# Performance work log

Hardware: AMD Instinct MI355X
Metric: run time of the kernel (lower is better)

## Reference

```python
import jax, jax.numpy as jnp
import numpy as np

B, T, C, H = 1, 2048, 1024, 16
HD = C // H
WIN = 256            # sliding_window_size
NLEV = 256           # quantization levels (input/weights/output)
CLAMP = 1.0          # clamping bounds [-1, 1] when quantization is active


def window_mask(n_tokens, win):
    i = jnp.arange(n_tokens)[:, None]
    j = jnp.arange(n_tokens)[None, :]
    return ((j <= i) & (j > i - win)).astype(jnp.float32)  # [T, T]


def quantize_ste(x, n_levels, vmin, vmax):
    # quantization_custom: q_step * round(x / q_step), straight-through gradient
    q_step = (vmax - vmin) / (n_levels - 1)
    q = q_step * jnp.round(x / q_step)
    return x + jax.lax.stop_gradient(q - x)


def setup_inputs() -> dict:
    key = jax.random.key(0)
    k0, k1, k2 = jax.random.split(key, 3)
    x = jax.random.normal(k0, (B, T, C), dtype=jnp.float32)
    w_attn = jax.random.normal(k1, (C, 3 * C), dtype=jnp.float32) * 0.02  # c_attn.weight (no bias)
    w_proj = jax.random.normal(k2, (C, C), dtype=jnp.float32) * 0.02      # c_proj.weight (no bias)
    return {"x": x, "w_attn": w_attn, "w_proj": w_proj}


def reference(x, w_attn, w_proj):
    # c_attn + split into per-head q,k,v -> [B,H,T,HD]
    qkv = x @ w_attn
    q, k, v = jnp.split(qkv, 3, axis=-1)
    to_heads = lambda t: t.reshape(B, T, H, HD).transpose(0, 2, 1, 3)
    q, k, v = to_heads(q), to_heads(k), to_heads(v)

    # range_scalers are identity here (a=1, b=0, not trainable); clamp + quantize (DAC simulation)
    q = quantize_ste(jnp.clip(q, -CLAMP, CLAMP), NLEV, -CLAMP, CLAMP)
    k = quantize_ste(jnp.clip(k, -CLAMP, CLAMP), NLEV, -CLAMP, CLAMP)
    v = quantize_ste(jnp.clip(v, -CLAMP, CLAMP), NLEV, -CLAMP, CLAMP)

    mask = window_mask(T, WIN)  # [T, T]

    # similarity = matmul: [B,H,T,T]
    att = jnp.einsum('bhqd,bhkd->bhqk', q, k)
    # masked_fill with mask_value_1 = 0.0, decay = Identity
    att = jnp.where(mask == 0, 0.0, att)
    # att_score_scaler: a = HD**-0.5
    att = att * (HD ** -0.5)
    # output clamp + quantization of analog array readout
    att = quantize_ste(jnp.clip(att, -CLAMP, CLAMP), NLEV, -CLAMP, CLAMP)
    # masked_fill with mask_value_2 = -inf, then softmax (NL)
    att = jnp.where(mask == 0, -jnp.inf, att)
    att = jax.nn.softmax(att, axis=-1)

    # weight_average = matmul: [B,H,T,HD]
    y = jnp.einsum('bhqk,bhkd->bhqd', att, v)
    # weight_average_scaler identity; output clamp + quantize; output_scaler identity
    y = quantize_ste(jnp.clip(y, -CLAMP, CLAMP), NLEV, -CLAMP, CLAMP)

    y = y.transpose(0, 2, 1, 3).reshape(B, T, C)
    y = y @ w_proj  # resid dropout p=0.0
    return y
```

## Files before the change

kernel.cpp:

```cpp
#include <hip/hip_runtime.h>

using u16 = unsigned short;
using u32 = unsigned int;

typedef __bf16 bf16x8 __attribute__((ext_vector_type(8)));
typedef float f32x4 __attribute__((ext_vector_type(4)));

#define T_SEQ 2048
#define NC 1024
#define HDIM 64
#define WINSZ 256
#define QSTEP (2.0f / 255.0f)

__device__ __forceinline__ float b2f(u16 u) {
  u32 v = ((u32)u) << 16;
  return __builtin_bit_cast(float, v);
}
__device__ __forceinline__ u16 f2b(float f) {
  u32 x = __builtin_bit_cast(u32, f);
  u32 r = (x + 0x7fffu + ((x >> 16) & 1u)) >> 16;
  return (u16)r;
}
__device__ __forceinline__ float quantize(float v) {
  v = fminf(fmaxf(v, -1.0f), 1.0f);
  return QSTEP * rintf(v / QSTEP);
}

__global__ __launch_bounds__(256) void k1_prep(const float* __restrict__ x, u16* __restrict__ xb,
                                               const float* __restrict__ wa, u16* __restrict__ wTa,
                                               const float* __restrict__ wp, u16* __restrict__ wTp) {
  if (blockIdx.z == 2) {
    const int nb = gridDim.x * gridDim.y;
    const int bid = blockIdx.y * gridDim.x + blockIdx.x;
    const int n4 = T_SEQ * NC / 4;
    for (int i = bid * 256 + threadIdx.x; i < n4; i += nb * 256) {
      const float4 v = ((const float4*)x)[i];
      ushort4 o;
      o.x = f2b(v.x); o.y = f2b(v.y); o.z = f2b(v.z); o.w = f2b(v.w);
      ((ushort4*)xb)[i] = o;
    }
    return;
  }
  const int iswp = (blockIdx.z == 1);
  if (iswp && blockIdx.x >= 16) return;
  const float* in = iswp ? wp : wa;
  u16* out = iswp ? wTp : wTa;
  const int Cc = iswp ? 1024 : 3072;
  __shared__ u16 tile[64][65];
  const int tc = blockIdx.x * 64, tr = blockIdx.y * 64;
  const int lx = threadIdx.x & 63, ly = threadIdx.x >> 6;
#pragma unroll
  for (int r = ly; r < 64; r += 4)
    tile[r][lx] = f2b(in[(long)(tr + r) * Cc + tc + lx]);
  __syncthreads();
  const int e = threadIdx.x & 31;
  const int r0 = (threadIdx.x >> 5) & 1;
  const int w = threadIdx.x >> 6;
#pragma unroll
  for (int it = 0; it < 8; it++) {
    const int r = it * 8 + w * 2 + r0;
    ushort2 o2;
    o2.x = tile[2 * e][r];
    o2.y = tile[2 * e + 1][r];
    *(ushort2*)&out[(tc + r) * 1024 + tr + 2 * e] = o2;
  }
}

__global__ __launch_bounds__(256, 3) void k2_qkv(const u16* __restrict__ A,
                                                 const u16* __restrict__ BT,
                                                 u16* __restrict__ o0, u16* __restrict__ o1,
                                                 u16* __restrict__ o2) {
  __shared__ __align__(16) u16 As[2][4096];
  __shared__ __align__(16) u16 Bs[2][8192];
  const int tid = threadIdx.x;
  const int lane = tid & 63;
  const int wave = tid >> 6;
  const int wr = wave >> 1, wc = wave & 1;
  const int ln15 = lane & 15, lq = lane >> 4;
  const int l7 = ln15 & 7;

  const int wg = blockIdx.y * 24 + blockIdx.x;
  const int xcd = wg & 7, t = wg >> 3;
  const int bx = (xcd & 1) * 12 + t % 12;
  const int by = (xcd >> 1) * 8 + t / 12;
  const int m0 = by * 64, n0 = bx * 128;

  const int crow = tid >> 3, csl = tid & 7;
  const u16* ag0 = A + (m0 + crow) * NC + csl * 8;
  const u16* bg0 = BT + (n0 + crow) * NC + csl * 8;
  const int wofs = crow * 64 + (csl ^ (crow & 7)) * 8;

  uint4 pa0, pa1, pb0, pb1, pb2, pb3;
  uint4 qa0, qa1, qb0, qb1, qb2, qb3;
  f32x4 acc[2][4] = {};

#define K2_LOADP(KT)                                  \
  {                                                   \
    pa0 = *(const uint4*)(ag0 + (KT));                \
    pa1 = *(const uint4*)(ag0 + 32 * NC + (KT));      \
    pb0 = *(const uint4*)(bg0 + (KT));                \
    pb1 = *(const uint4*)(bg0 + 32 * NC + (KT));      \
    pb2 = *(const uint4*)(bg0 + 64 * NC + (KT));      \
    pb3 = *(const uint4*)(bg0 + 96 * NC + (KT));      \
  }
#define K2_LOADQ(KT)                                  \
  {                                                   \
    qa0 = *(const uint4*)(ag0 + (KT));                \
    qa1 = *(const uint4*)(ag0 + 32 * NC + (KT));      \
    qb0 = *(const uint4*)(bg0 + (KT));                \
    qb1 = *(const uint4*)(bg0 + 32 * NC + (KT));      \
    qb2 = *(const uint4*)(bg0 + 64 * NC + (KT));      \
    qb3 = *(const uint4*)(bg0 + 96 * NC + (KT));      \
  }
#define K2_WRITEP(BUF)                                \
  {                                                   \
    *(uint4*)&As[BUF][wofs] = pa0;                    \
    *(uint4*)&As[BUF][wofs + 2048] = pa1;             \
    *(uint4*)&Bs[BUF][wofs] = pb0;                    \
    *(uint4*)&Bs[BUF][wofs + 2048] = pb1;             \
    *(uint4*)&Bs[BUF][wofs + 4096] = pb2;             \
    *(uint4*)&Bs[BUF][wofs + 6144] = pb3;             \
  }
#define K2_WRITEQ(BUF)                                \
  {                                                   \
    *(uint4*)&As[BUF][wofs] = qa0;                    \
    *(uint4*)&As[BUF][wofs + 2048] = qa1;             \
    *(uint4*)&Bs[BUF][wofs] = qb0;                    \
    *(uint4*)&Bs[BUF][wofs + 2048] = qb1;             \
    *(uint4*)&Bs[BUF][wofs + 4096] = qb2;             \
    *(uint4*)&Bs[BUF][wofs + 6144] = qb3;             \
  }

  auto compute = [&](const u16* LA, const u16* LB) {
#pragma unroll
    for (int s = 0; s < 2; s++) {
      const int kc = s * 4 + lq;
      const int sw = kc ^ l7;
      bf16x8 af[2], bfr[4];
#pragma unroll
      for (int r = 0; r < 2; r++) {
        const int ar = wr * 32 + r * 16 + ln15;
        af[r] = *(const bf16x8*)&LA[(ar * 8 + sw) * 8];
      }
#pragma unroll
      for (int c = 0; c < 4; c++) {
        const int br = wc * 64 + c * 16 + ln15;
        bfr[c] = *(const bf16x8*)&LB[(br * 8 + sw) * 8];
      }
#pragma unroll
      for (int r = 0; r < 2; r++)
#pragma unroll
        for (int c = 0; c < 4; c++)
          acc[r][c] = __builtin_amdgcn_mfma_f32_16x16x32_bf16(af[r], bfr[c], acc[r][c], 0, 0, 0);
    }
  };

  K2_LOADP(0);
  K2_WRITEP(0);
  K2_LOADQ(64);

  for (int kt = 0; kt < NC; kt += 128) {
    __syncthreads();
    if (kt + 128 < NC) K2_LOADP(kt + 128);
    compute(As[0], Bs[0]);
    K2_WRITEQ(1);
    __syncthreads();
    if (kt + 192 < NC) K2_LOADQ(kt + 192);
    compute(As[1], Bs[1]);
    if (kt + 128 < NC) K2_WRITEP(0);
  }
#undef K2_LOADP
#undef K2_LOADQ
#undef K2_WRITEP
#undef K2_WRITEQ

#pragma unroll
  for (int c = 0; c < 4; c++) {
    const int gcol = n0 + wc * 64 + c * 16 + ln15;
    const int p = gcol >> 10;
    const int h = (gcol & 1023) >> 6;
    const int hd = gcol & 63;
#pragma unroll
    for (int r = 0; r < 2; r++) {
      const int rbase = m0 + wr * 32 + r * 16 + lq * 4;
#pragma unroll
      for (int g = 0; g < 4; g++) {
        const u16 b = f2b(quantize(acc[r][c][g]));
        const int row = rbase + g;
        if (p == 0)      o0[(h * T_SEQ + row) * HDIM + hd] = b;
        else if (p == 1) o1[(h * T_SEQ + row) * HDIM + hd] = b;
        else             o2[(h * HDIM + hd) * T_SEQ + row] = b;
      }
    }
  }
}

__global__ __launch_bounds__(256, 4) void k3_attn(const u16* __restrict__ qh,
                                                  const u16* __restrict__ kh,
                                                  const u16* __restrict__ vt,
                                                  u16* __restrict__ yq) {
  __shared__ __align__(16) u16 S[32 * 328];
  __shared__ float Linv[32];
  const int tid = threadIdx.x;
  const int lane = tid & 63;
  const int wave = tid >> 6;
  const int ln15 = lane & 15, lq = lane >> 4;

  const int g = blockIdx.y * 64 + blockIdx.x;
  const int lin = (g & 7) * 128 + (g >> 3);
  const int h = lin >> 6;
  const int i0 = (lin & 63) * 32;
  const int j0 = i0 - 256;

  const u16* qb = qh + (h * T_SEQ + i0) * HDIM;
  const u16* kb = kh + h * T_SEQ * HDIM;

  bf16x8 qf[2][2];
#pragma unroll
  for (int r = 0; r < 2; r++) {
    qf[r][0] = *(const bf16x8*)&qb[(r * 16 + ln15) * HDIM + lq * 8];
    qf[r][1] = *(const bf16x8*)&qb[(r * 16 + ln15) * HDIM + 32 + lq * 8];
  }

  bf16x8 kf[5][2];
#pragma unroll
  for (int t = 0; t < 5; t++) {
    const int jt = j0 + (wave + t * 4) * 16;
    if (jt >= 0 && jt <= T_SEQ - 16) {
      kf[t][0] = *(const bf16x8*)&kb[(jt + ln15) * HDIM + lq * 8];
      kf[t][1] = *(const bf16x8*)&kb[(jt + ln15) * HDIM + 32 + lq * 8];
    } else {
      kf[t][0] = bf16x8{};
      kf[t][1] = bf16x8{};
    }
  }

#pragma unroll
  for (int t = 0; t < 5; t++) {
    const int ct = wave + t * 4;
    const int jt = j0 + ct * 16;
#pragma unroll
    for (int rt = 0; rt < 2; rt++) {
      const bool skip = (ct < rt) || (ct > rt + 16) || (jt < 0);
      f32x4 s = {0.f, 0.f, 0.f, 0.f};
      if (!skip) {
        __builtin_amdgcn_s_setprio(1);
        s = __builtin_amdgcn_mfma_f32_16x16x32_bf16(kf[t][0], qf[rt][0], s, 0, 0, 0);
        s = __builtin_amdgcn_mfma_f32_16x16x32_bf16(kf[t][1], qf[rt][1], s, 0, 0, 0);
        __builtin_amdgcn_s_setprio(0);
      }
      const int i = i0 + rt * 16 + ln15;
      ushort4 pk;
      u16* pp = (u16*)&pk;
#pragma unroll
      for (int g2 = 0; g2 < 4; g2++) {
        const int j = jt + lq * 4 + g2;
        float v = -INFINITY;
        if (!skip && j <= i && j > i - WINSZ) v = quantize(s[g2] * 0.125f);
        pp[g2] = f2b(v);
      }
      *(ushort4*)&S[(rt * 16 + ln15) * 328 + ct * 16 + lq * 4] = pk;
    }
  }

  const u16* vb = vt + (h * HDIM + wave * 16 + ln15) * T_SEQ;
  bf16x8 vf[9];
#pragma unroll
  for (int kk = 0; kk < 9; kk++) {
    int jb = j0 + kk * 32 + lq * 8;
    if (jb < 0) jb = 0;
    vf[kk] = *(const bf16x8*)&vb[jb];
  }
  __syncthreads();

  {
    const int r = tid >> 3, sg = tid & 7;
    u16* Srow = &S[r * 328 + sg * 40];
    uint4 ch[5];
    float m = -INFINITY;
#pragma unroll
    for (int c = 0; c < 5; c++) {
      ch[c] = *(const uint4*)&Srow[c * 8];
      const u32* w = (const u32*)&ch[c];
#pragma unroll
      for (int d = 0; d < 4; d++) {
        m = fmaxf(m, b2f((u16)(w[d] & 0xffffu)));
        m = fmaxf(m, b2f((u16)(w[d] >> 16)));
      }
    }
    m = fmaxf(m, __shfl_xor(m, 1));
    m = fmaxf(m, __shfl_xor(m, 2));
    m = fmaxf(m, __shfl_xor(m, 4));
    float l = 0.0f;
#pragma unroll
    for (int c = 0; c < 5; c++) {
      u32* w = (u32*)&ch[c];
#pragma unroll
      for (int d = 0; d < 4; d++) {
        const float e0 = __expf(b2f((u16)(w[d] & 0xffffu)) - m);
        const float e1 = __expf(b2f((u16)(w[d] >> 16)) - m);
        l += e0 + e1;
        w[d] = ((u32)f2b(e1) << 16) | f2b(e0);
      }
      *(uint4*)&Srow[c * 8] = ch[c];
    }
    l += __shfl_xor(l, 1);
    l += __shfl_xor(l, 2);
    l += __shfl_xor(l, 4);
    if (sg == 0) Linv[r] = 1.0f / l;
  }
  __syncthreads();

  f32x4 acc[2] = {};
#pragma unroll
  for (int kk = 0; kk < 9; kk++) {
#pragma unroll
    for (int rt = 0; rt < 2; rt++) {
      const bf16x8 pf = *(const bf16x8*)&S[(rt * 16 + ln15) * 328 + kk * 32 + lq * 8];
      __builtin_amdgcn_s_setprio(1);
      acc[rt] = __builtin_amdgcn_mfma_f32_16x16x32_bf16(pf, vf[kk], acc[rt], 0, 0, 0);
      __builtin_amdgcn_s_setprio(0);
    }
  }
#pragma unroll
  for (int rt = 0; rt < 2; rt++)
#pragma unroll
    for (int g2 = 0; g2 < 4; g2++) {
      const int row = rt * 16 + lq * 4 + g2;
      const int i = i0 + row;
      yq[i * NC + h * HDIM + wave * 16 + ln15] = f2b(quantize(acc[rt][g2] * Linv[row]));
    }
}

__global__ __launch_bounds__(256, 4) void k4_proj(const u16* __restrict__ A,
                                                  const u16* __restrict__ BT,
                                                  float* __restrict__ of) {
  __shared__ __align__(16) u16 As[2][4096];
  __shared__ __align__(16) u16 Bs[2][4096];
  const int tid = threadIdx.x;
  const int lane = tid & 63;
  const int wave = tid >> 6;
  const int wr = wave >> 1, wc = wave & 1;
  const int ln15 = lane & 15, lq = lane >> 4;
  const int l7 = ln15 & 7;

  const int wg = blockIdx.y * 16 + blockIdx.x;
  const int xcd = wg & 7, t = wg >> 3;
  const int bx = (xcd & 1) * 8 + t % 8;
  const int by = (xcd >> 1) * 8 + t / 8;
  const int m0 = by * 64, n0 = bx * 64;

  const int crow = tid >> 3, csl = tid & 7;
  const u16* ag0 = A + (m0 + crow) * NC + csl * 8;
  const u16* bg0 = BT + (n0 + crow) * NC + csl * 8;
  const int wofs = crow * 64 + (csl ^ (crow & 7)) * 8;

  uint4 pa0, pa1, pb0, pb1;
  uint4 qa0, qa1, qb0, qb1;
  f32x4 acc[2][2] = {};

#define K4_LOADP(KT)                               \
  {                                                \
    pa0 = *(const uint4*)(ag0 + (KT));             \
    pa1 = *(const uint4*)(ag0 + 32 * NC + (KT));   \
    pb0 = *(const uint4*)(bg0 + (KT));             \
    pb1 = *(const uint4*)(bg0 + 32 * NC + (KT));   \
  }
#define K4_LOADQ(KT)                               \
  {                                                \
    qa0 = *(const uint4*)(ag0 + (KT));             \
    qa1 = *(const uint4*)(ag0 + 32 * NC + (KT));   \
    qb0 = *(const uint4*)(bg0 + (KT));             \
    qb1 = *(const uint4*)(bg0 + 32 * NC + (KT));   \
  }
#define K4_WRITEP(BUF)                             \
  {                                                \
    *(uint4*)&As[BUF][wofs] = pa0;                 \
    *(uint4*)&As[BUF][wofs + 2048] = pa1;          \
    *(uint4*)&Bs[BUF][wofs] = pb0;                 \
    *(uint4*)&Bs[BUF][wofs + 2048] = pb1;          \
  }
#define K4_WRITEQ(BUF)                             \
  {                                                \
    *(uint4*)&As[BUF][wofs] = qa0;                 \
    *(uint4*)&As[BUF][wofs + 2048] = qa1;          \
    *(uint4*)&Bs[BUF][wofs] = qb0;                 \
    *(uint4*)&Bs[BUF][wofs + 2048] = qb1;          \
  }

  auto compute = [&](const u16* LA, const u16* LB) {
#pragma unroll
    for (int s = 0; s < 2; s++) {
      const int kc = s * 4 + lq;
      const int sw = kc ^ l7;
      bf16x8 af[2], bfr[2];
#pragma unroll
      for (int r = 0; r < 2; r++) {
        const int ar = wr * 32 + r * 16 + ln15;
        af[r] = *(const bf16x8*)&LA[(ar * 8 + sw) * 8];
      }
#pragma unroll
      for (int c = 0; c < 2; c++) {
        const int br = wc * 32 + c * 16 + ln15;
        bfr[c] = *(const bf16x8*)&LB[(br * 8 + sw) * 8];
      }
#pragma unroll
      for (int r = 0; r < 2; r++)
#pragma unroll
        for (int c = 0; c < 2; c++)
          acc[r][c] = __builtin_amdgcn_mfma_f32_16x16x32_bf16(af[r], bfr[c], acc[r][c], 0, 0, 0);
    }
  };

  K4_LOADP(0);
  K4_WRITEP(0);
  K4_LOADQ(64);

  for (int kt = 0; kt < NC; kt += 128) {
    __syncthreads();
    if (kt + 128 < NC) K4_LOADP(kt + 128);
    compute(As[0], Bs[0]);
    K4_WRITEQ(1);
    __syncthreads();
    if (kt + 192 < NC) K4_LOADQ(kt + 192);
    compute(As[1], Bs[1]);
    if (kt + 128 < NC) K4_WRITEP(0);
  }
#undef K4_LOADP
#undef K4_LOADQ
#undef K4_WRITEP
#undef K4_WRITEQ

#pragma unroll
  for (int r = 0; r < 2; r++)
#pragma unroll
    for (int g = 0; g < 4; g++) {
      const int row = m0 + wr * 32 + r * 16 + lq * 4 + g;
#pragma unroll
      for (int c = 0; c < 2; c++)
        of[(long)row * NC + n0 + wc * 32 + c * 16 + ln15] = acc[r][c][g];
    }
}

extern "C" void kernel_launch(void* const* d_in, const int* in_sizes, int n_in,
                              void* d_out, int out_size, void* d_ws, size_t ws_size,
                              hipStream_t stream) {
  const void *px = d_in[0], *pwa = d_in[1], *pwp = d_in[2];
  for (int i = 0; i < n_in; i++) {
    if (in_sizes[i] == 2048 * 1024) px = d_in[i];
    else if (in_sizes[i] == 3072 * 1024) pwa = d_in[i];
    else if (in_sizes[i] == 1024 * 1024) pwp = d_in[i];
  }

  char* ws = (char*)d_ws;
  u16* xb  = (u16*)(ws + (1u << 20));
  u16* wTa = (u16*)(ws + (5u << 20));
  u16* wTp = (u16*)(ws + (11u << 20));
  u16* qh  = (u16*)(ws + (13u << 20));
  u16* kh  = (u16*)(ws + (17u << 20));
  u16* vt  = (u16*)(ws + (21u << 20));
  u16* yq  = (u16*)(ws + (25u << 20));

  k1_prep<<<dim3(48, 16, 3), 256, 0, stream>>>((const float*)px, xb, (const float*)pwa, wTa,
                                               (const float*)pwp, wTp);
  k2_qkv<<<dim3(24, 32), 256, 0, stream>>>(xb, wTa, qh, kh, vt);
  k3_attn<<<dim3(64, 16), 256, 0, stream>>>(qh, kh, vt, yq);
  k4_proj<<<dim3(16, 32), 256, 0, stream>>>(yq, wTp, (float*)d_out);
}
```

Before: 124.7 us.

## Fuse four kernels into one persistent cooperative kernel with grid syncs

Replaces the four separate launches (prep, QKV GEMM, windowed attention, projection) with a single cooperative kernel of 768 blocks. The phases are separated by grid.sync(), and each phase loops its block indices over the persistent grid. This removes kernel launch gaps and tail effects between stages. The cost is grid-wide barrier latency, launch bounds of 3 blocks per CU that may limit registers, and idle blocks in the projection phase. If the cooperative launch fails, the code falls back to the original four launches.

```diff
diff --git a/kernel.cpp b/kernel.cpp
--- a/kernel.cpp
+++ b/kernel.cpp
@@ -1,4 +1,7 @@
 #include <hip/hip_runtime.h>
+#include <hip/hip_cooperative_groups.h>
+
+namespace cg = cooperative_groups;
 
 using u16 = unsigned short;
 using u32 = unsigned int;
@@ -26,6 +29,363 @@
   return QSTEP * rintf(v / QSTEP);
 }
 
+__global__ __launch_bounds__(256, 3) void fused(
+    const float* __restrict__ xf, u16* __restrict__ xb,
+    const float* __restrict__ wa, u16* __restrict__ wTa,
+    const float* __restrict__ wp, u16* __restrict__ wTp,
+    u16* __restrict__ qh, u16* __restrict__ kh, u16* __restrict__ vt,
+    u16* __restrict__ yq, float* __restrict__ out) {
+  cg::grid_group grid = cg::this_grid();
+  __shared__ __align__(16) union {
+    struct { u16 As[4096]; u16 Bs[8192]; } g2;
+    struct { u16 S[32 * 328]; float Linv[32]; } at;
+    struct { u16 As[4096]; u16 Bs[4096]; } g4;
+    u16 tile[64][65];
+  } sh;
+
+  const int b = blockIdx.x;
+  const int tid = threadIdx.x;
+  const int lane = tid & 63;
+  const int wave = tid >> 6;
+  const int ln15 = lane & 15, lq = lane >> 4;
+  const int l7 = ln15 & 7;
+
+  {
+    const int n4 = T_SEQ * NC / 4;
+    for (int i = b * 256 + tid; i < n4; i += 768 * 256) {
+      const float4 v = ((const float4*)xf)[i];
+      ushort4 o;
+      o.x = f2b(v.x); o.y = f2b(v.y); o.z = f2b(v.z); o.w = f2b(v.w);
+      ((ushort4*)xb)[i] = o;
+    }
+    for (int j = b; j < 1024; j += 768) {
+      __syncthreads();
+      const int iswp = (j >= 768);
+      const int bi = iswp ? (j - 768) : j;
+      const float* in = iswp ? wp : wa;
+      u16* outw = iswp ? wTp : wTa;
+      const int Cc = iswp ? 1024 : 3072;
+      const int W = iswp ? 16 : 48;
+      const int tc = (bi % W) * 64, tr = (bi / W) * 64;
+      const int lx = tid & 63, ly = tid >> 6;
+#pragma unroll
+      for (int r = ly; r < 64; r += 4)
+        sh.tile[r][lx] = f2b(in[(long)(tr + r) * Cc + tc + lx]);
+      __syncthreads();
+      const int e = tid & 31;
+      const int r0 = (tid >> 5) & 1;
+#pragma unroll
+      for (int it = 0; it < 8; it++) {
+        const int r = it * 8 + wave * 2 + r0;
+        ushort2 o2;
+        o2.x = sh.tile[2 * e][r];
+        o2.y = sh.tile[2 * e + 1][r];
+        *(ushort2*)&outw[(tc + r) * 1024 + tr + 2 * e] = o2;
+      }
+    }
+  }
+  grid.sync();
+
+  {
+    const int wr = wave >> 1, wc = wave & 1;
+    const int xcd = b & 7, tt = b >> 3;
+    const int bx = (xcd & 1) * 12 + tt % 12;
+    const int by = (xcd >> 1) * 8 + tt / 12;
+    const int m0 = by * 64, n0 = bx * 128;
+
+    const int crow = tid >> 3, csl = tid & 7;
+    const u16* ag0 = xb + (m0 + crow) * NC + csl * 8;
+    const u16* bg0 = wTa + (n0 + crow) * NC + csl * 8;
+    const int wofs = crow * 64 + (csl ^ (crow & 7)) * 8;
+
+    uint4 pa0, pa1, pb0, pb1, pb2, pb3;
+    f32x4 acc[2][4] = {};
+
+#define K2_LOAD(KT)                                 \
+  {                                                 \
+    pa0 = *(const uint4*)(ag0 + (KT));              \
+    pa1 = *(const uint4*)(ag0 + 32 * NC + (KT));    \
+    pb0 = *(const uint4*)(bg0 + (KT));              \
+    pb1 = *(const uint4*)(bg0 + 32 * NC + (KT));    \
+    pb2 = *(const uint4*)(bg0 + 64 * NC + (KT));    \
+    pb3 = *(const uint4*)(bg0 + 96 * NC + (KT));    \
+  }
+#define K2_WRITE()                                  \
+  {                                                 \
+    *(uint4*)&sh.g2.As[wofs] = pa0;                 \
+    *(uint4*)&sh.g2.As[wofs + 2048] = pa1;          \
+    *(uint4*)&sh.g2.Bs[wofs] = pb0;                 \
+    *(uint4*)&sh.g2.Bs[wofs + 2048] = pb1;          \
+    *(uint4*)&sh.g2.Bs[wofs + 4096] = pb2;          \
+    *(uint4*)&sh.g2.Bs[wofs + 6144] = pb3;          \
+  }
+
+    __syncthreads();
+    K2_LOAD(0);
+    K2_WRITE();
+    __syncthreads();
+
+    for (int kt = 0; kt < NC; kt += 64) {
+      if (kt + 64 < NC) K2_LOAD(kt + 64);
+#pragma unroll
+      for (int s = 0; s < 2; s++) {
+        const int kc = s * 4 + lq;
+        const int sw = kc ^ l7;
+        bf16x8 af[2], bfr[4];
+#pragma unroll
+        for (int r = 0; r < 2; r++) {
+          const int ar = wr * 32 + r * 16 + ln15;
+          af[r] = *(const bf16x8*)&sh.g2.As[(ar * 8 + sw) * 8];
+        }
+#pragma unroll
+        for (int c = 0; c < 4; c++) {
+          const int br = wc * 64 + c * 16 + ln15;
+          bfr[c] = *(const bf16x8*)&sh.g2.Bs[(br * 8 + sw) * 8];
+        }
+#pragma unroll
+        for (int r = 0; r < 2; r++)
+#pragma unroll
+          for (int c = 0; c < 4; c++)
+            acc[r][c] = __builtin_amdgcn_mfma_f32_16x16x32_bf16(af[r], bfr[c], acc[r][c], 0, 0, 0);
+      }
+      if (kt + 64 < NC) {
+        __syncthreads();
+        K2_WRITE();
+        __syncthreads();
+      }
+    }
+#undef K2_LOAD
+#undef K2_WRITE
+
+#pragma unroll
+    for (int c = 0; c < 4; c++) {
+      const int gcol = n0 + wc * 64 + c * 16 + ln15;
+      const int p = gcol >> 10;
+      const int h = (gcol & 1023) >> 6;
+      const int hd = gcol & 63;
+#pragma unroll
+      for (int r = 0; r < 2; r++) {
+        const int rbase = m0 + wr * 32 + r * 16 + lq * 4;
+#pragma unroll
+        for (int g = 0; g < 4; g++) {
+          const u16 bq = f2b(quantize(acc[r][c][g]));
+          const int row = rbase + g;
+          if (p == 0)      qh[(h * T_SEQ + row) * HDIM + hd] = bq;
+          else if (p == 1) kh[(h * T_SEQ + row) * HDIM + hd] = bq;
+          else             vt[(h * HDIM + hd) * T_SEQ + row] = bq;
+        }
+      }
+    }
+  }
+  grid.sync();
+
+  for (int ga = b; ga < 1024; ga += 768) {
+    __syncthreads();
+    const int lin = (ga & 7) * 128 + (ga >> 3);
+    const int h = lin >> 6;
+    const int i0 = (lin & 63) * 32;
+    const int j0 = i0 - 256;
+
+    const u16* qb = qh + (h * T_SEQ + i0) * HDIM;
+    const u16* kb = kh + h * T_SEQ * HDIM;
+
+    bf16x8 qf[2][2];
+#pragma unroll
+    for (int r = 0; r < 2; r++) {
+      qf[r][0] = *(const bf16x8*)&qb[(r * 16 + ln15) * HDIM + lq * 8];
+      qf[r][1] = *(const bf16x8*)&qb[(r * 16 + ln15) * HDIM + 32 + lq * 8];
+    }
+
+    bf16x8 kf[5][2];
+#pragma unroll
+    for (int t = 0; t < 5; t++) {
+      const int jt = j0 + (wave + t * 4) * 16;
+      if (jt >= 0 && jt <= T_SEQ - 16) {
+        kf[t][0] = *(const bf16x8*)&kb[(jt + ln15) * HDIM + lq * 8];
+        kf[t][1] = *(const bf16x8*)&kb[(jt + ln15) * HDIM + 32 + lq * 8];
+      } else {
+        kf[t][0] = bf16x8{};
+        kf[t][1] = bf16x8{};
+      }
+    }
+
+#pragma unroll
+    for (int t = 0; t < 5; t++) {
+      const int ct = wave + t * 4;
+      const int jt = j0 + ct * 16;
+#pragma unroll
+      for (int rt = 0; rt < 2; rt++) {
+        const bool skip = (ct < rt) || (ct > rt + 16) || (jt < 0);
+        f32x4 s = {0.f, 0.f, 0.f, 0.f};
+        if (!skip) {
+          __builtin_amdgcn_s_setprio(1);
+          s = __builtin_amdgcn_mfma_f32_16x16x32_bf16(kf[t][0], qf[rt][0], s, 0, 0, 0);
+          s = __builtin_amdgcn_mfma_f32_16x16x32_bf16(kf[t][1], qf[rt][1], s, 0, 0, 0);
+          __builtin_amdgcn_s_setprio(0);
+        }
+        const int i = i0 + rt * 16 + ln15;
+        ushort4 pk;
+        u16* pp = (u16*)&pk;
+#pragma unroll
+        for (int g2 = 0; g2 < 4; g2++) {
+          const int j = jt + lq * 4 + g2;
+          float v = -INFINITY;
+          if (!skip && j <= i && j > i - WINSZ) v = quantize(s[g2] * 0.125f);
+          pp[g2] = f2b(v);
+        }
+        *(ushort4*)&sh.at.S[(rt * 16 + ln15) * 328 + ct * 16 + lq * 4] = pk;
+      }
+    }
+
+    const u16* vb = vt + (h * HDIM + wave * 16 + ln15) * T_SEQ;
+    bf16x8 vf[9];
+#pragma unroll
+    for (int kk = 0; kk < 9; kk++) {
+      int jb = j0 + kk * 32 + lq * 8;
+      if (jb < 0) jb = 0;
+      vf[kk] = *(const bf16x8*)&vb[jb];
+    }
+    __syncthreads();
+
+    {
+      const int r = tid >> 3, sg = tid & 7;
+      u16* Srow = &sh.at.S[r * 328 + sg * 40];
+      uint4 ch[5];
+      float m = -INFINITY;
+#pragma unroll
+      for (int c = 0; c < 5; c++) {
+        ch[c] = *(const uint4*)&Srow[c * 8];
+        const u32* w = (const u32*)&ch[c];
+#pragma unroll
+        for (int d = 0; d < 4; d++) {
+          m = fmaxf(m, b2f((u16)(w[d] & 0xffffu)));
+          m = fmaxf(m, b2f((u16)(w[d] >> 16)));
+        }
+      }
+      m = fmaxf(m, __shfl_xor(m, 1));
+      m = fmaxf(m, __shfl_xor(m, 2));
+      m = fmaxf(m, __shfl_xor(m, 4));
+      float l = 0.0f;
+#pragma unroll
+      for (int c = 0; c < 5; c++) {
+        u32* w = (u32*)&ch[c];
+#pragma unroll
+        for (int d = 0; d < 4; d++) {
+          const float e0 = __expf(b2f((u16)(w[d] & 0xffffu)) - m);
+          const float e1 = __expf(b2f((u16)(w[d] >> 16)) - m);
+          l += e0 + e1;
+          w[d] = ((u32)f2b(e1) << 16) | f2b(e0);
+        }
+        *(uint4*)&Srow[c * 8] = ch[c];
+      }
+      l += __shfl_xor(l, 1);
+      l += __shfl_xor(l, 2);
+      l += __shfl_xor(l, 4);
+      if (sg == 0) sh.at.Linv[r] = 1.0f / l;
+    }
+    __syncthreads();
+
+    f32x4 acc[2] = {};
+#pragma unroll
+    for (int kk = 0; kk < 9; kk++) {
+#pragma unroll
+      for (int rt = 0; rt < 2; rt++) {
+        const bf16x8 pf = *(const bf16x8*)&sh.at.S[(rt * 16 + ln15) * 328 + kk * 32 + lq * 8];
+        __builtin_amdgcn_s_setprio(1);
+        acc[rt] = __builtin_amdgcn_mfma_f32_16x16x32_bf16(pf, vf[kk], acc[rt], 0, 0, 0);
+        __builtin_amdgcn_s_setprio(0);
+      }
+    }
+#pragma unroll
+    for (int rt = 0; rt < 2; rt++)
+#pragma unroll
+      for (int g2 = 0; g2 < 4; g2++) {
+        const int row = rt * 16 + lq * 4 + g2;
+        const int i = i0 + row;
+        yq[i * NC + h * HDIM + wave * 16 + ln15] = f2b(quantize(acc[rt][g2] * sh.at.Linv[row]));
+      }
+  }
+  grid.sync();
+
+  if (b < 512) {
+    const int wr = wave >> 1, wc = wave & 1;
+    const int xcd = b & 7, tt = b >> 3;
+    const int bx = (xcd & 1) * 8 + tt % 8;
+    const int by = (xcd >> 1) * 8 + tt / 8;
+    const int m0 = by * 64, n0 = bx * 64;
+
+    const int crow = tid >> 3, csl = tid & 7;
+    const u16* ag0 = yq + (m0 + crow) * NC + csl * 8;
+    const u16* bg0 = wTp + (n0 + crow) * NC + csl * 8;
+    const int wofs = crow * 64 + (csl ^ (crow & 7)) * 8;
+
+    uint4 pa0, pa1, pb0, pb1;
+    f32x4 acc[2][2] = {};
+
+#define K4_LOAD(KT)                                 \
+  {                                                 \
+    pa0 = *(const uint4*)(ag0 + (KT));              \
+    pa1 = *(const uint4*)(ag0 + 32 * NC + (KT));    \
+    pb0 = *(const uint4*)(bg0 + (KT));              \
+    pb1 = *(const uint4*)(bg0 + 32 * NC + (KT));    \
+  }
+#define K4_WRITE()                                  \
+  {                                                 \
+    *(uint4*)&sh.g4.As[wofs] = pa0;                 \
+    *(uint4*)&sh.g4.As[wofs + 2048] = pa1;          \
+    *(uint4*)&sh.g4.Bs[wofs] = pb0;                 \
+    *(uint4*)&sh.g4.Bs[wofs + 2048] = pb1;          \
+  }
+
+    __syncthreads();
+    K4_LOAD(0);
+    K4_WRITE();
+    __syncthreads();
+
+    for (int kt = 0; kt < NC; kt += 64) {
+      if (kt + 64 < NC) K4_LOAD(kt + 64);
+#pragma unroll
+      for (int s = 0; s < 2; s++) {
+        const int kc = s * 4 + lq;
+        const int sw = kc ^ l7;
+        bf16x8 af[2], bfr[2];
+#pragma unroll
+        for (int r = 0; r < 2; r++) {
+          const int ar = wr * 32 + r * 16 + ln15;
+          af[r] = *(const bf16x8*)&sh.g4.As[(ar * 8 + sw) * 8];
+        }
+#pragma unroll
+        for (int c = 0; c < 2; c++) {
+          const int br = wc * 32 + c * 16 + ln15;
+          bfr[c] = *(const bf16x8*)&sh.g4.Bs[(br * 8 + sw) * 8];
+        }
+#pragma unroll
+        for (int r = 0; r < 2; r++)
+#pragma unroll
+          for (int c = 0; c < 2; c++)
+            acc[r][c] = __builtin_amdgcn_mfma_f32_16x16x32_bf16(af[r], bfr[c], acc[r][c], 0, 0, 0);
+      }
+      if (kt + 64 < NC) {
+        __syncthreads();
+        K4_WRITE();
+        __syncthreads();
+      }
+    }
+#undef K4_LOAD
+#undef K4_WRITE
+
+#pragma unroll
+    for (int r = 0; r < 2; r++)
+#pragma unroll
+      for (int g = 0; g < 4; g++) {
+        const int row = m0 + wr * 32 + r * 16 + lq * 4 + g;
+#pragma unroll
+        for (int c = 0; c < 2; c++)
+          out[(long)row * NC + n0 + wc * 32 + c * 16 + ln15] = acc[r][c][g];
+      }
+  }
+}
+
 __global__ __launch_bounds__(256) void k1_prep(const float* __restrict__ x, u16* __restrict__ xb,
                                                const float* __restrict__ wa, u16* __restrict__ wTa,
                                                const float* __restrict__ wp, u16* __restrict__ wTp) {
@@ -461,9 +821,27 @@
   u16* vt  = (u16*)(ws + (21u << 20));
   u16* yq  = (u16*)(ws + (25u << 20));
 
-  k1_prep<<<dim3(48, 16, 3), 256, 0, stream>>>((const float*)px, xb, (const float*)pwa, wTa,
-                                               (const float*)pwp, wTp);
-  k2_qkv<<<dim3(24, 32), 256, 0, stream>>>(xb, wTa, qh, kh, vt);
-  k3_attn<<<dim3(64, 16), 256, 0, stream>>>(qh, kh, vt, yq);
-  k4_proj<<<dim3(16, 32), 256, 0, stream>>>(yq, wTp, (float*)d_out);
+  const float* a0 = (const float*)px;
+  u16* a1 = xb;
+  const float* a2 = (const float*)pwa;
+  u16* a3 = wTa;
+  const float* a4 = (const float*)pwp;
+  u16* a5 = wTp;
+  u16* a6 = qh;
+  u16* a7 = kh;
+  u16* a8 = vt;
+  u16* a9 = yq;
+  float* a10 = (float*)d_out;
+  void* args[] = {&a0, &a1, &a2, &a3, &a4, &a5, &a6, &a7, &a8, &a9, &a10};
+
+  hipError_t rc = hipLaunchCooperativeKernel(reinterpret_cast<const void*>(&fused), dim3(768),
+                                             dim3(256), args, 0, stream);
+  if (rc != hipSuccess) {
+    (void)hipGetLastError();
+    k1_prep<<<dim3(48, 16, 3), 256, 0, stream>>>((const float*)px, xb, (const float*)pwa, wTa,
+                                                 (const float*)pwp, wTp);
+    k2_qkv<<<dim3(24, 32), 256, 0, stream>>>(xb, wTa, qh, kh, vt);
+    k3_attn<<<dim3(64, 16), 256, 0, stream>>>(qh, kh, vt, yq);
+    k4_proj<<<dim3(16, 32), 256, 0, stream>>>(yq, wTp, (float*)d_out);
+  }
 }
```

New measurement: 409.8 us. +228.6%, slower.
